# Kernel optimization log

Hardware: AMD Instinct MI355X
Metric: run time of the kernel (lower is better)

## Reference

```python
import jax, jax.numpy as jnp
import numpy as np

N = 1_048_576      # flattened batch (forward reshapes to (-1, 4))
Q_DIM = 4
HIDDEN = 64
DC = Q_DIM // 2    # q_dim_changed = 2
NUM_LO = (DC * DC - DC) // 2  # = 1
SLOPE = 0.01       # torch leaky_relu default negative slope


def setup_inputs() -> dict:
    key = jax.random.key(0)
    ks = jax.random.split(key, 9)
    def lin(kw, kb, fan_out, fan_in):
        bound = 1.0 / np.sqrt(fan_in)
        W = jax.random.uniform(kw, (fan_out, fan_in), jnp.float32, -bound, bound)
        b = jax.random.uniform(kb, (fan_out,), jnp.float32, -bound, bound)
        return W, b
    x = jax.random.normal(ks[0], (N, Q_DIM), jnp.float32)
    W1, b1 = lin(ks[1], ks[2], HIDDEN, Q_DIM)
    W2, b2 = lin(ks[3], ks[4], HIDDEN, HIDDEN)
    W_Ld, b_Ld = lin(ks[5], ks[6], DC, HIDDEN)
    W_Lo, b_Lo = lin(ks[7], ks[8], NUM_LO, HIDDEN)
    return {"x": x, "W1": W1, "b1": b1, "W2": W2, "b2": b2,
            "W_Ld": W_Ld, "b_Ld": b_Ld, "W_Lo": W_Lo, "b_Lo": b_Lo}


def reference(x, W1, b1, W2, b2, W_Ld, b_Ld, W_Lo, b_Lo):
    q = x.reshape(-1, Q_DIM)                      # (n, 4)
    n = q.shape[0]
    h1 = jax.nn.leaky_relu(q @ W1.T + b1, SLOPE)  # (n, 64)
    h2 = jax.nn.leaky_relu(h1 @ W2.T + b2, SLOPE) # (n, 64); dropout is eval-mode identity
    Ld = jax.nn.softplus(h2 @ W_Ld.T + b_Ld)      # (n, 2) positive diagonal
    Lo = h2 @ W_Lo.T + b_Lo                       # (n, 1) strictly-lower entries
    rows, cols = jnp.tril_indices(DC, -1)         # strictly lower triangle, row-major
    diag = jnp.arange(DC)
    L = jnp.zeros((n, DC, DC), dtype=q.dtype)
    L = L.at[:, rows, cols].set(Lo)               # scatter Lo (matches torch boolean-mask fill order)
    L = L.at[:, diag, diag].set(Ld)               # diag_embed(Ld)
    H = jnp.einsum('nij,nkj->nik', L, L) + 1e-9 * jnp.eye(DC, dtype=q.dtype)
    return H
```

## Files before the change

### kernel.cpp

```cpp
#include <hip/hip_runtime.h>


typedef __attribute__((ext_vector_type(8))) short bf16x8;
typedef __attribute__((ext_vector_type(4))) float f32x4;

#define ROWS_PER_BLOCK 256
#define H_STRIDE 72
#define LDS_SHORTS (ROWS_PER_BLOCK * H_STRIDE)

__device__ __forceinline__ float lrelu(float a) {
    return fmaxf(a, 0.01f * a);
}

__device__ __forceinline__ float softplus(float v) {
    return fmaxf(v, 0.0f) + log1pf(expf(-fabsf(v)));
}

__device__ __forceinline__ unsigned short bf16_rne(float f) {
    unsigned u = __float_as_uint(f);
    u += 0x7FFFu + ((u >> 16) & 1u);
    return (unsigned short)(u >> 16);
}

__device__ __forceinline__ unsigned pk_bf16(float lo, float hi) {
    return (unsigned)bf16_rne(lo) | ((unsigned)bf16_rne(hi) << 16);
}

__global__ __launch_bounds__(256) void dln_mfma(
    const float* __restrict__ x,
    const float* __restrict__ W1,  const float* __restrict__ b1,
    const float* __restrict__ W2,  const float* __restrict__ b2,
    const float* __restrict__ WLd, const float* __restrict__ bLd,
    const float* __restrict__ WLo, const float* __restrict__ bLo,
    float* __restrict__ out)
{
    __shared__ __align__(16) unsigned short lds[LDS_SHORTS];

    const int tid  = threadIdx.x;
    const int lane = tid & 63;
    const int wv   = tid >> 6;
    const int quad = lane >> 4;
    const int col  = lane & 15;

    {
        const float4* src = (const float4*)W2;
        float4*       dst = (float4*)lds;
#pragma unroll
        for (int i = 0; i < 4; ++i)
            dst[tid + 256 * i] = src[tid + 256 * i];
    }
    float b2c[4];
#pragma unroll
    for (int t = 0; t < 4; ++t) b2c[t] = b2[16 * t + col];
    __syncthreads();

    bf16x8 bfrag[4][2];
    {
        const float* w2l = (const float*)lds;
#pragma unroll
        for (int t = 0; t < 4; ++t) {
#pragma unroll
            for (int s = 0; s < 2; ++s) {
                const float* p = w2l + (16 * t + col) * 64 + 32 * s + 8 * quad;
                float4 f0 = *(const float4*)(p);
                float4 f1 = *(const float4*)(p + 4);
                uint4 u;
                u.x = pk_bf16(f0.x, f0.y);
                u.y = pk_bf16(f0.z, f0.w);
                u.z = pk_bf16(f1.x, f1.y);
                u.w = pk_bf16(f1.z, f1.w);
                bfrag[t][s] = __builtin_bit_cast(bf16x8, u);
            }
        }
    }
    __syncthreads();

    const int row_g = blockIdx.x * ROWS_PER_BLOCK + tid;
    {
        const float4 qv = ((const float4*)x)[row_g];
        unsigned short* myrow = lds + tid * H_STRIDE;
#pragma unroll
        for (int blk = 0; blk < 8; ++blk) {
            unsigned up[4];
#pragma unroll
            for (int p = 0; p < 4; ++p) {
                float h[2];
#pragma unroll
                for (int e = 0; e < 2; ++e) {
                    const int j = blk * 8 + p * 2 + e;
                    float a = b1[j];
                    a = fmaf(qv.x, W1[4 * j + 0], a);
                    a = fmaf(qv.y, W1[4 * j + 1], a);
                    a = fmaf(qv.z, W1[4 * j + 2], a);
                    a = fmaf(qv.w, W1[4 * j + 3], a);
                    h[e] = lrelu(a);
                }
                up[p] = pk_bf16(h[0], h[1]);
            }
            *(uint4*)(myrow + blk * 8) = make_uint4(up[0], up[1], up[2], up[3]);
        }
    }

#pragma unroll
    for (int mt = 0; mt < 4; ++mt) {
        const int rbase = wv * 64 + mt * 16;
        const unsigned short* ar = lds + (rbase + col) * H_STRIDE + 8 * quad;
        uint4 a0u = *(const uint4*)(ar);
        uint4 a1u = *(const uint4*)(ar + 32);
        bf16x8 a0 = __builtin_bit_cast(bf16x8, a0u);
        bf16x8 a1 = __builtin_bit_cast(bf16x8, a1u);

        f32x4 acc[4];
#pragma unroll
        for (int t = 0; t < 4; ++t) {
            acc[t] = (f32x4){b2c[t], b2c[t], b2c[t], b2c[t]};
            acc[t] = __builtin_amdgcn_mfma_f32_16x16x32_bf16(a0, bfrag[t][0], acc[t], 0, 0, 0);
            acc[t] = __builtin_amdgcn_mfma_f32_16x16x32_bf16(a1, bfrag[t][1], acc[t], 0, 0, 0);
        }
#pragma unroll
        for (int t = 0; t < 4; ++t) {
#pragma unroll
            for (int r = 0; r < 4; ++r) {
                const float v = lrelu(acc[t][r]);
                lds[(rbase + quad * 4 + r) * H_STRIDE + 16 * t + col] = bf16_rne(v);
            }
        }
    }
    __syncthreads();

    {
        const unsigned short* hr = lds + tid * H_STRIDE;
        float ld0 = bLd[0];
        float ld1 = bLd[1];
        float lo  = bLo[0];
#pragma unroll
        for (int i = 0; i < 8; ++i) {
            const uint4 u = *(const uint4*)(hr + i * 8);
            const unsigned uu[4] = {u.x, u.y, u.z, u.w};
#pragma unroll
            for (int p = 0; p < 4; ++p) {
                const int k = i * 8 + p * 2;
                const float e0 = __uint_as_float(uu[p] << 16);
                const float e1 = __uint_as_float(uu[p] & 0xFFFF0000u);
                ld0 = fmaf(e0, WLd[k],          ld0);
                ld0 = fmaf(e1, WLd[k + 1],      ld0);
                ld1 = fmaf(e0, WLd[64 + k],     ld1);
                ld1 = fmaf(e1, WLd[64 + k + 1], ld1);
                lo  = fmaf(e0, WLo[k],          lo);
                lo  = fmaf(e1, WLo[k + 1],      lo);
            }
        }
        ld0 = softplus(ld0);
        ld1 = softplus(ld1);
        float4 o;
        o.x = fmaf(ld0, ld0, 1e-9f);
        o.y = ld0 * lo;
        o.z = o.y;
        o.w = fmaf(lo, lo, fmaf(ld1, ld1, 1e-9f));
        reinterpret_cast<float4*>(out)[row_g] = o;
    }
}

__global__ __launch_bounds__(256) void dln_tail(
    const float* __restrict__ x,
    const float* __restrict__ W1,  const float* __restrict__ b1,
    const float* __restrict__ W2,  const float* __restrict__ b2,
    const float* __restrict__ WLd, const float* __restrict__ bLd,
    const float* __restrict__ WLo, const float* __restrict__ bLo,
    float* __restrict__ out, int row0, int nrows)
{
    const int row = row0 + blockIdx.x * 256 + threadIdx.x;
    if (row >= nrows) return;
    const float4 qv = reinterpret_cast<const float4*>(x)[row];
    float h1[64];
#pragma unroll
    for (int j = 0; j < 64; ++j) {
        float a = b1[j];
        a = fmaf(qv.x, W1[4 * j + 0], a);
        a = fmaf(qv.y, W1[4 * j + 1], a);
        a = fmaf(qv.z, W1[4 * j + 2], a);
        a = fmaf(qv.w, W1[4 * j + 3], a);
        h1[j] = lrelu(a);
    }
    float ld0 = bLd[0], ld1 = bLd[1], lo = bLo[0];
#pragma unroll 4
    for (int j = 0; j < 64; ++j) {
        float a0 = b2[j], a1 = 0.0f;
        const float* w = W2 + 64 * j;
#pragma unroll
        for (int k = 0; k < 64; k += 2) {
            a0 = fmaf(h1[k],     w[k],     a0);
            a1 = fmaf(h1[k + 1], w[k + 1], a1);
        }
        const float a = lrelu(a0 + a1);
        ld0 = fmaf(a, WLd[j],      ld0);
        ld1 = fmaf(a, WLd[64 + j], ld1);
        lo  = fmaf(a, WLo[j],      lo);
    }
    ld0 = softplus(ld0);
    ld1 = softplus(ld1);
    float4 o;
    o.x = fmaf(ld0, ld0, 1e-9f);
    o.y = ld0 * lo;
    o.z = o.y;
    o.w = fmaf(lo, lo, fmaf(ld1, ld1, 1e-9f));
    reinterpret_cast<float4*>(out)[row] = o;
}

extern "C" void kernel_launch(void* const* d_in, const int* in_sizes, int n_in,
                              void* d_out, int out_size, void* d_ws, size_t ws_size,
                              hipStream_t stream)
{
    const float* x   = (const float*)d_in[0];
    const float* W1  = (const float*)d_in[1];
    const float* b1  = (const float*)d_in[2];
    const float* W2  = (const float*)d_in[3];
    const float* b2  = (const float*)d_in[4];
    const float* WLd = (const float*)d_in[5];
    const float* bLd = (const float*)d_in[6];
    const float* WLo = (const float*)d_in[7];
    const float* bLo = (const float*)d_in[8];
    float* out = (float*)d_out;

    const int nrows = in_sizes[0] / 4;
    const int nfull = nrows / ROWS_PER_BLOCK;
    const int rem   = nrows - nfull * ROWS_PER_BLOCK;

    if (nfull > 0)
        dln_mfma<<<nfull, 256, 0, stream>>>(
            x, W1, b1, W2, b2, WLd, bLd, WLo, bLo, out);
    if (rem > 0)
        dln_tail<<<(rem + 255) / 256, 256, 0, stream>>>(
            x, W1, b1, W2, b2, WLd, bLd, WLo, bLo, out,
            nfull * ROWS_PER_BLOCK, nrows);
}
```

Baseline: 131.1 us.

## Transpose MFMA so W2 is A operand and fuse head projection in registers

Measured after the change: 129.4 us. Within noise of the previous version (-1.3%).

```diff
diff --git a/kernel.cpp b/kernel.cpp
--- a/kernel.cpp
+++ b/kernel.cpp
@@ -5,8 +5,6 @@
 typedef __attribute__((ext_vector_type(4))) float f32x4;
 
 #define ROWS_PER_BLOCK 256
-#define H_STRIDE 72
-#define LDS_SHORTS (ROWS_PER_BLOCK * H_STRIDE)
 
 __device__ __forceinline__ float lrelu(float a) {
     return fmaxf(a, 0.01f * a);
@@ -16,17 +14,13 @@
     return fmaxf(v, 0.0f) + log1pf(expf(-fabsf(v)));
 }
 
-__device__ __forceinline__ unsigned short bf16_rne(float f) {
-    unsigned u = __float_as_uint(f);
-    u += 0x7FFFu + ((u >> 16) & 1u);
-    return (unsigned short)(u >> 16);
+__device__ __forceinline__ unsigned cvt_pk_bf16(float lo, float hi) {
+    unsigned r;
+    asm("v_cvt_pk_bf16_f32 %0, %1, %2" : "=v"(r) : "v"(lo), "v"(hi));
+    return r;
 }
 
-__device__ __forceinline__ unsigned pk_bf16(float lo, float hi) {
-    return (unsigned)bf16_rne(lo) | ((unsigned)bf16_rne(hi) << 16);
-}
-
-__global__ __launch_bounds__(256) void dln_mfma(
+__global__ __launch_bounds__(256, 3) void dln_mfma(
     const float* __restrict__ x,
     const float* __restrict__ W1,  const float* __restrict__ b1,
     const float* __restrict__ W2,  const float* __restrict__ b2,
@@ -34,60 +28,49 @@
     const float* __restrict__ WLo, const float* __restrict__ bLo,
     float* __restrict__ out)
 {
-    __shared__ __align__(16) unsigned short lds[LDS_SHORTS];
+    __shared__ __align__(16) unsigned short h1s[4][8][64][8];
 
     const int tid  = threadIdx.x;
     const int lane = tid & 63;
     const int wv   = tid >> 6;
     const int quad = lane >> 4;
-    const int col  = lane & 15;
+    const int c    = lane & 15;
 
-    {
-        const float4* src = (const float4*)W2;
-        float4*       dst = (float4*)lds;
+    bf16x8 afrag[4][2];
+    f32x4 wld0[4], wld1[4], wlo[4], b2v[4];
 #pragma unroll
-        for (int i = 0; i < 4; ++i)
-            dst[tid + 256 * i] = src[tid + 256 * i];
+    for (int mt = 0; mt < 4; ++mt) {
+        const float* wr = W2 + (16 * mt + c) * 64 + 8 * quad;
+#pragma unroll
+        for (int s = 0; s < 2; ++s) {
+            const float4 f0 = *(const float4*)(wr + 32 * s);
+            const float4 f1 = *(const float4*)(wr + 32 * s + 4);
+            uint4 u;
+            u.x = cvt_pk_bf16(f0.x, f0.y);
+            u.y = cvt_pk_bf16(f0.z, f0.w);
+            u.z = cvt_pk_bf16(f1.x, f1.y);
+            u.w = cvt_pk_bf16(f1.z, f1.w);
+            afrag[mt][s] = __builtin_bit_cast(bf16x8, u);
+        }
+        const int nb = 16 * mt + 4 * quad;
+        wld0[mt] = *(const f32x4*)(WLd + nb);
+        wld1[mt] = *(const f32x4*)(WLd + 64 + nb);
+        wlo[mt]  = *(const f32x4*)(WLo + nb);
+        b2v[mt]  = *(const f32x4*)(b2 + nb);
     }
-    float b2c[4];
-#pragma unroll
-    for (int t = 0; t < 4; ++t) b2c[t] = b2[16 * t + col];
-    __syncthreads();
-
-    bf16x8 bfrag[4][2];
-    {
-        const float* w2l = (const float*)lds;
-#pragma unroll
-        for (int t = 0; t < 4; ++t) {
-#pragma unroll
-            for (int s = 0; s < 2; ++s) {
-                const float* p = w2l + (16 * t + col) * 64 + 32 * s + 8 * quad;
-                float4 f0 = *(const float4*)(p);
-                float4 f1 = *(const float4*)(p + 4);
-                uint4 u;
-                u.x = pk_bf16(f0.x, f0.y);
-                u.y = pk_bf16(f0.z, f0.w);
-                u.z = pk_bf16(f1.x, f1.y);
-                u.w = pk_bf16(f1.z, f1.w);
-                bfrag[t][s] = __builtin_bit_cast(bf16x8, u);
-            }
-        }
-    }
-    __syncthreads();
 
     const int row_g = blockIdx.x * ROWS_PER_BLOCK + tid;
     {
         const float4 qv = ((const float4*)x)[row_g];
-        unsigned short* myrow = lds + tid * H_STRIDE;
 #pragma unroll
-        for (int blk = 0; blk < 8; ++blk) {
+        for (int ch = 0; ch < 8; ++ch) {
             unsigned up[4];
 #pragma unroll
             for (int p = 0; p < 4; ++p) {
                 float h[2];
 #pragma unroll
                 for (int e = 0; e < 2; ++e) {
-                    const int j = blk * 8 + p * 2 + e;
+                    const int j = ch * 8 + p * 2 + e;
                     float a = b1[j];
                     a = fmaf(qv.x, W1[4 * j + 0], a);
                     a = fmaf(qv.y, W1[4 * j + 1], a);
@@ -95,63 +78,42 @@
                     a = fmaf(qv.w, W1[4 * j + 3], a);
                     h[e] = lrelu(a);
                 }
-                up[p] = pk_bf16(h[0], h[1]);
+                up[p] = cvt_pk_bf16(h[0], h[1]);
             }
-            *(uint4*)(myrow + blk * 8) = make_uint4(up[0], up[1], up[2], up[3]);
+            *(uint4*)&h1s[wv][ch][lane][0] = make_uint4(up[0], up[1], up[2], up[3]);
         }
     }
 
+    float sld0 = 0.0f, sld1 = 0.0f, slo = 0.0f;
 #pragma unroll
-    for (int mt = 0; mt < 4; ++mt) {
-        const int rbase = wv * 64 + mt * 16;
-        const unsigned short* ar = lds + (rbase + col) * H_STRIDE + 8 * quad;
-        uint4 a0u = *(const uint4*)(ar);
-        uint4 a1u = *(const uint4*)(ar + 32);
-        bf16x8 a0 = __builtin_bit_cast(bf16x8, a0u);
-        bf16x8 a1 = __builtin_bit_cast(bf16x8, a1u);
+    for (int it = 0; it < 4; ++it) {
+        const bf16x8 b0 = *(const bf16x8*)&h1s[wv][quad][it * 16 + c][0];
+        const bf16x8 b1f = *(const bf16x8*)&h1s[wv][4 + quad][it * 16 + c][0];
 
-        f32x4 acc[4];
+        float pld0 = 0.0f, pld1 = 0.0f, plo = 0.0f;
 #pragma unroll
-        for (int t = 0; t < 4; ++t) {
-            acc[t] = (f32x4){b2c[t], b2c[t], b2c[t], b2c[t]};
-            acc[t] = __builtin_amdgcn_mfma_f32_16x16x32_bf16(a0, bfrag[t][0], acc[t], 0, 0, 0);
-            acc[t] = __builtin_amdgcn_mfma_f32_16x16x32_bf16(a1, bfrag[t][1], acc[t], 0, 0, 0);
-        }
-#pragma unroll
-        for (int t = 0; t < 4; ++t) {
+        for (int mt = 0; mt < 4; ++mt) {
+            f32x4 acc = b2v[mt];
+            acc = __builtin_amdgcn_mfma_f32_16x16x32_bf16(afrag[mt][0], b0, acc, 0, 0, 0);
+            acc = __builtin_amdgcn_mfma_f32_16x16x32_bf16(afrag[mt][1], b1f, acc, 0, 0, 0);
 #pragma unroll
             for (int r = 0; r < 4; ++r) {
-                const float v = lrelu(acc[t][r]);
-                lds[(rbase + quad * 4 + r) * H_STRIDE + 16 * t + col] = bf16_rne(v);
+                const float h2 = lrelu(acc[r]);
+                pld0 = fmaf(h2, wld0[mt][r], pld0);
+                pld1 = fmaf(h2, wld1[mt][r], pld1);
+                plo  = fmaf(h2, wlo[mt][r],  plo);
             }
         }
+        pld0 += __shfl_xor(pld0, 16); pld0 += __shfl_xor(pld0, 32);
+        pld1 += __shfl_xor(pld1, 16); pld1 += __shfl_xor(pld1, 32);
+        plo  += __shfl_xor(plo,  16); plo  += __shfl_xor(plo,  32);
+        if (it == quad) { sld0 = pld0; sld1 = pld1; slo = plo; }
     }
-    __syncthreads();
 
     {
-        const unsigned short* hr = lds + tid * H_STRIDE;
-        float ld0 = bLd[0];
-        float ld1 = bLd[1];
-        float lo  = bLo[0];
-#pragma unroll
-        for (int i = 0; i < 8; ++i) {
-            const uint4 u = *(const uint4*)(hr + i * 8);
-            const unsigned uu[4] = {u.x, u.y, u.z, u.w};
-#pragma unroll
-            for (int p = 0; p < 4; ++p) {
-                const int k = i * 8 + p * 2;
-                const float e0 = __uint_as_float(uu[p] << 16);
-                const float e1 = __uint_as_float(uu[p] & 0xFFFF0000u);
-                ld0 = fmaf(e0, WLd[k],          ld0);
-                ld0 = fmaf(e1, WLd[k + 1],      ld0);
-                ld1 = fmaf(e0, WLd[64 + k],     ld1);
-                ld1 = fmaf(e1, WLd[64 + k + 1], ld1);
-                lo  = fmaf(e0, WLo[k],          lo);
-                lo  = fmaf(e1, WLo[k + 1],      lo);
-            }
-        }
-        ld0 = softplus(ld0);
-        ld1 = softplus(ld1);
+        const float ld0 = softplus(sld0 + bLd[0]);
+        const float ld1 = softplus(sld1 + bLd[1]);
+        const float lo  = slo + bLo[0];
         float4 o;
         o.x = fmaf(ld0, ld0, 1e-9f);
         o.y = ld0 * lo;
```
